# Optimization experiments

Measured on AMD Instinct MI355X. Metric: run time of the kernel, lower is better.

## Reference

```python
import jax, jax.numpy as jnp
import numpy as np

MIX_TIME = 20
NUM_SAMPLES = 128
NUM_ONES = 64


def setup_inputs() -> dict:
    key = jax.random.key(0)
    kz, ka, kw = jax.random.split(key, 3)
    B, D, DZ = 128, 512, 512
    z = (jax.random.uniform(kz, (B, DZ)) < 0.5).astype(jnp.float32)  # conditioned binary vars
    A = jax.random.normal(ka, (D, D), dtype=jnp.float32) * 0.02      # pairwise couplings
    W = jax.random.normal(kw, (D, DZ), dtype=jnp.float32) * 0.02     # w-z couplings
    return {"z": z, "A": A, "W": W}


def reference(z, A, W):
    # Batched conditional double-flip Gibbs sampler.
    # State x: (S, B, D) binary floats; per step pick distinct coords (i, j),
    # evaluate unnormalized log p(w|z) for the 4 value combos, sample categorically.
    S = NUM_SAMPLES
    B, DZ = z.shape
    D = A.shape[0]

    x0 = jnp.zeros((S, B, D), dtype=jnp.float32).at[..., :NUM_ONES].set(1.0)
    cond = jnp.broadcast_to(z[None], (S, B, DZ))  # (S,B,DZ)

    def logp(w):  # quadratic energy: w^T A w + w^T W z  -> (S,B)
        return (jnp.einsum('sbd,de,sbe->sb', w, A, w)
                + jnp.einsum('sbd,dk,sbk->sb', w, W, cond))

    combos = jnp.array([[0., 0.], [0., 1.], [1., 0.], [1., 1.]], dtype=jnp.float32)

    def step(x, k):
        ki, ks = jax.random.split(k)
        ij = jax.random.choice(ki, D, (2,), replace=False)  # distinct i, j
        i, j = ij[0], ij[1]

        def set_ij(v):  # clone x with coords (i,j) set to (v0, v1)
            return x.at[..., i].set(v[0]).at[..., j].set(v[1])

        xs = jax.vmap(set_ij)(combos)                    # (4,S,B,D)
        logits = jnp.moveaxis(jax.vmap(logp)(xs), 0, -1)  # (S,B,4)
        samp = jax.random.categorical(ks, logits)         # (S,B) in {0,1,2,3}
        iv = (samp // 2).astype(x.dtype)
        jv = (samp % 2).astype(x.dtype)
        x = x.at[..., i].set(iv).at[..., j].set(jv)
        return x, None

    keys = jax.random.split(jax.random.key(1), MIX_TIME)
    x, _ = jax.lax.scan(step, x0, keys)
    return x
```

## Files before the change

### kernel.cpp

```cpp
#include <hip/hip_runtime.h>
#include <stdint.h>

#define MIX_TIME 20
#define NCHAIN   16384
#define DDIM     512

#define WS_TBL 0
#define WS_SC  128
#define WS_T0  288
#define WS_U0  800
#define WS_ST0 1312
#define WS_SZ0 1344
#define WS_C   1472

struct U2 { uint32_t a, b; };

__device__ __forceinline__ uint32_t rotl32(uint32_t v, int r) {
  return (v << r) | (v >> (32 - r));
}

__device__ __forceinline__ U2 tf2x32(uint32_t k0, uint32_t k1, uint32_t x0, uint32_t x1) {
  const uint32_t ks2 = k0 ^ k1 ^ 0x1BD11BDAu;
  x0 += k0; x1 += k1;
  x0 += x1; x1 = rotl32(x1, 13); x1 ^= x0;
  x0 += x1; x1 = rotl32(x1, 15); x1 ^= x0;
  x0 += x1; x1 = rotl32(x1, 26); x1 ^= x0;
  x0 += x1; x1 = rotl32(x1,  6); x1 ^= x0;
  x0 += k1; x1 += ks2 + 1u;
  x0 += x1; x1 = rotl32(x1, 17); x1 ^= x0;
  x0 += x1; x1 = rotl32(x1, 29); x1 ^= x0;
  x0 += x1; x1 = rotl32(x1, 16); x1 ^= x0;
  x0 += x1; x1 = rotl32(x1, 24); x1 ^= x0;
  x0 += ks2; x1 += k0 + 2u;
  x0 += x1; x1 = rotl32(x1, 13); x1 ^= x0;
  x0 += x1; x1 = rotl32(x1, 15); x1 ^= x0;
  x0 += x1; x1 = rotl32(x1, 26); x1 ^= x0;
  x0 += x1; x1 = rotl32(x1,  6); x1 ^= x0;
  x0 += k0; x1 += k1 + 3u;
  x0 += x1; x1 = rotl32(x1, 17); x1 ^= x0;
  x0 += x1; x1 = rotl32(x1, 29); x1 ^= x0;
  x0 += x1; x1 = rotl32(x1, 16); x1 ^= x0;
  x0 += x1; x1 = rotl32(x1, 24); x1 ^= x0;
  x0 += k1; x1 += ks2 + 4u;
  x0 += x1; x1 = rotl32(x1, 13); x1 ^= x0;
  x0 += x1; x1 = rotl32(x1, 15); x1 ^= x0;
  x0 += x1; x1 = rotl32(x1, 26); x1 ^= x0;
  x0 += x1; x1 = rotl32(x1,  6); x1 ^= x0;
  x0 += ks2; x1 += k0 + 5u;
  return {x0, x1};
}

__device__ __forceinline__ uint32_t rbits32(uint32_t k0, uint32_t k1, uint32_t m) {
  U2 r = tf2x32(k0, k1, 0u, m);
  return r.a ^ r.b;
}
__device__ __forceinline__ U2 split_key(uint32_t k0, uint32_t k1, uint32_t idx) {
  return tf2x32(k0, k1, 0u, idx);
}

__device__ __forceinline__ float gumbel_from(uint32_t bits) {
  float u = __uint_as_float(0x3f800000u | (bits >> 9)) - 1.0f;
  u = fmaxf(u + 1.17549435e-38f, 1.17549435e-38f);
  return -logf(-logf(u));
}

__device__ __forceinline__ float bpermf(int byteidx, float v) {
  return __int_as_float(__builtin_amdgcn_ds_bpermute(byteidx, __float_as_int(v)));
}
__device__ __forceinline__ uint32_t bpermu(int byteidx, uint32_t v) {
  return (uint32_t)__builtin_amdgcn_ds_bpermute(byteidx, (int)v);
}

__global__ __launch_bounds__(256)
void pre_kernel(const float* __restrict__ A, const float* __restrict__ W,
                const float* __restrict__ z, uint32_t* __restrict__ wsu,
                float* __restrict__ wsf) {
  const int bid = blockIdx.x, tid = threadIdx.x;
  uint32_t* tbl = wsu + WS_TBL;
  uint32_t* sc  = wsu + WS_SC;
  float* T0  = wsf + WS_T0;
  float* U0  = wsf + WS_U0;
  float* St0 = wsf + WS_ST0;
  float* Sz0 = wsf + WS_SZ0;
  float* C   = wsf + WS_C;

  __shared__ float  sred[64];
  __shared__ float4 zs4[8][128];
  __shared__ float  credL[8][64];

  if (bid < MIX_TIME) {
    if (tid >= 64) return;
    const uint32_t t    = (uint32_t)bid;
    const uint32_t lane = (uint32_t)tid;
    const U2 K   = split_key(0u, 1u, t);
    const U2 ki  = split_key(K.a, K.b, 0u);
    const U2 ks  = split_key(K.a, K.b, 1u);
    const U2 sub = split_key(ki.a, ki.b, 1u);

    uint32_t k1 = 0xFFFFFFFFu, m1 = 0xFFFFFFFFu;
    uint32_t k2 = 0xFFFFFFFFu, m2 = 0xFFFFFFFFu;
    #pragma unroll
    for (int p = 0; p < 8; ++p) {
      const uint32_t m   = lane + 64u * (uint32_t)p;
      const uint32_t key = rbits32(sub.a, sub.b, m);
      const bool lt1 = (key < k1) || (key == k1 && m < m1);
      const bool lt2 = (key < k2) || (key == k2 && m < m2);
      if (lt1)      { k2 = k1; m2 = m1; k1 = key; m1 = m; }
      else if (lt2) { k2 = key; m2 = m; }
    }
    #pragma unroll
    for (int msk = 1; msk < 64; msk <<= 1) {
      const uint32_t ok1 = __shfl_xor((int)k1, msk, 64);
      const uint32_t om1 = __shfl_xor((int)m1, msk, 64);
      const uint32_t ok2 = __shfl_xor((int)k2, msk, 64);
      const uint32_t om2 = __shfl_xor((int)m2, msk, 64);
      const bool oless = (ok1 < k1) || (ok1 == k1 && om1 < m1);
      if (oless) {
        const bool l2 = (k1 < ok2) || (k1 == ok2 && m1 < om2);
        const uint32_t nk2 = l2 ? k1 : ok2, nm2 = l2 ? m1 : om2;
        k1 = ok1; m1 = om1; k2 = nk2; m2 = nm2;
      } else {
        const bool l2 = (ok1 < k2) || (ok1 == k2 && om1 < m2);
        if (l2) { k2 = ok1; m2 = om1; }
      }
    }
    if (lane == 0) {
      tbl[4u * t + 0u] = m1;
      tbl[4u * t + 1u] = m2;
      tbl[4u * t + 2u] = ks.a;
      tbl[4u * t + 3u] = ks.b;
      sc[8u * t + 0u] = m1;
      sc[8u * t + 1u] = m2;
      sc[8u * t + 6u] = 0u;
      sc[8u * t + 7u] = 0u;
    }
    if (lane < 4) {
      const uint32_t r = (lane < 2) ? m1 : m2;
      const uint32_t c = (lane & 1) ? m2 : m1;
      sc[8u * t + 2u + lane] = __float_as_uint(A[(size_t)r * DDIM + c]);
    }
    return;
  }

  if (bid <= MIX_TIME + 1) {
    const int e = (bid - MIX_TIME) * 256 + tid;
    float s = 0.f;
    #pragma unroll 1
    for (int d = 0; d < 64; ++d) s += A[(size_t)d * DDIM + e];
    T0[e] = s;
    if (bid == MIX_TIME) {
      if (tid < 64) sred[tid] = s;
      __syncthreads();
      if (tid == 0) {
        float q = 0.f;
        #pragma unroll 1
        for (int e2 = 0; e2 < 64; ++e2) q += sred[e2];
        St0[0] = q;
      }
    }
    return;
  }

  if (bid <= MIX_TIME + 3) {
    const int d = (bid - MIX_TIME - 2) * 256 + tid;
    const float4* Ar = reinterpret_cast<const float4*>(A + (size_t)d * DDIM);
    float s = 0.f;
    #pragma unroll
    for (int k = 0; k < 16; ++k) {
      const float4 v = Ar[k];
      s += v.x; s += v.y; s += v.z; s += v.w;
    }
    U0[d] = s;
    return;
  }

  const int cb = bid - (MIX_TIME + 4);
  const int bg = cb >> 3, slab = cb & 7;
  #pragma unroll
  for (int k = 0; k < 4; ++k) {
    const int idx = tid + 256 * k;
    const int br = idx >> 7, c4i = idx & 127;
    zs4[br][c4i] = reinterpret_cast<const float4*>(z + (size_t)(bg * 8 + br) * DDIM)[c4i];
  }
  __syncthreads();
  const int r = tid & 63;
  const int h = tid >> 6;
  const int d = slab * 64 + r;
  const float4* Wr = reinterpret_cast<const float4*>(W + (size_t)d * DDIM);
  float s0 = 0.f, s1 = 0.f;
  #pragma unroll 4
  for (int k = 0; k < 128; ++k) {
    const float4 w = Wr[k];
    const float4 za = zs4[2 * h][k], zb = zs4[2 * h + 1][k];
    s0 = fmaf(w.x, za.x, s0); s0 = fmaf(w.y, za.y, s0);
    s0 = fmaf(w.z, za.z, s0); s0 = fmaf(w.w, za.w, s0);
    s1 = fmaf(w.x, zb.x, s1); s1 = fmaf(w.y, zb.y, s1);
    s1 = fmaf(w.z, zb.z, s1); s1 = fmaf(w.w, zb.w, s1);
  }
  C[(size_t)(bg * 8 + 2 * h) * DDIM + d]     = s0;
  C[(size_t)(bg * 8 + 2 * h + 1) * DDIM + d] = s1;
  if (slab == 0) { credL[2 * h][r] = s0; credL[2 * h + 1][r] = s1; }
  __syncthreads();
  if (slab == 0 && tid < 8) {
    float s = 0.f;
    #pragma unroll 1
    for (int e = 0; e < 64; ++e) s += credL[tid][e];
    Sz0[bg * 8 + tid] = s;
  }
}

__global__ __launch_bounds__(256)
void gibbs8_kernel(const float* __restrict__ A,
                   const uint32_t* __restrict__ wsu,
                   const float* __restrict__ wsf,
                   float* __restrict__ out) {
  const int tid = threadIdx.x;
  const int l = tid & 63, wv = tid >> 6;
  const uint32_t* tbl = wsu + WS_TBL;
  const uint32_t* sc  = wsu + WS_SC;
  const float* T0w  = wsf + WS_T0;
  const float* U0w  = wsf + WS_U0;
  const float* St0w = wsf + WS_ST0;
  const float* Sz0w = wsf + WS_SZ0;
  const float* Cw   = wsf + WS_C;

  __shared__ __align__(16) float gg[3200];
  __shared__ uint32_t tblL[80];
  if (tid < 80) tblL[tid] = tbl[tid];
  __syncthreads();
  #pragma unroll 1
  for (int p = tid; p < 1600; p += 256) {
    const int r = p / 40, c = p % 40;
    const uint32_t cr = tblL[4 * (r >> 1) + (r & 1)];
    const uint32_t cc = tblL[4 * (c >> 1) + (c & 1)];
    gg[p]        = A[(size_t)cr * DDIM + cc];
    gg[1600 + p] = A[(size_t)cc * DDIM + cr];
  }

  const int ql = l >> 3, qs = l & 7, c4 = l & 3;
  const uint32_t chainbase = ((uint32_t)blockIdx.x * 4u + (uint32_t)wv) * 8u;
  const uint32_t chain_l = chainbase + (uint32_t)ql;
  const uint32_t b_l = chain_l & 127u;
  const uint32_t b_s = (chainbase + (uint32_t)qs) & 127u;
  const float fa  = (float)((c4 >> 1) & 1);
  const float fb  = (float)(c4 & 1);
  const float fab = fa * fb;

  float fTi[3], fTj[3], fUi[3], fUj[3], fci[3], fcj[3], fxi[3], fxj[3];
  uint32_t iiK[3], jjK[3];
  const float* ggb[3];
  #pragma unroll
  for (int k = 0; k < 3; ++k) {
    const int tp = (64 * k + l) >> 3;
    const int tc = (tp < MIX_TIME) ? tp : 0;
    const uint32_t i = sc[8 * tc], j = sc[8 * tc + 1];
    iiK[k] = i; jjK[k] = j;
    fTi[k] = T0w[i];  fTj[k] = T0w[j];
    fUi[k] = U0w[i];  fUj[k] = U0w[j];
    fci[k] = Cw[(size_t)b_s * DDIM + i];
    fcj[k] = Cw[(size_t)b_s * DDIM + j];
    fxi[k] = (i < 64u) ? 1.f : 0.f;
    fxj[k] = (j < 64u) ? 1.f : 0.f;
    ggb[k] = &gg[2 * tc];
  }
  float St = St0w[0];
  float Sz = Sz0w[b_l];
  uint32_t mlo = (qs == 0) ? 0xFFFFFFFFu : 0u;
  uint32_t mhi = mlo;

  float garr[10];
  #pragma unroll
  for (int k = 0; k < 10; ++k) {
    const int f = 64 * k + l;
    const int t = f >> 5;
    const uint32_t qg = ((uint32_t)l & 31u) >> 2;
    const uint32_t m  = (chainbase + qg) * 4u + (uint32_t)(l & 3);
    garr[k] = gumbel_from(rbits32(tbl[4 * t + 2], tbl[4 * t + 3], m));
  }
  __syncthreads();

  const int gvbase = (4 * ql + c4) << 2;
  const int bq4    = ql << 2;

  #pragma unroll
  for (int t = 0; t < MIX_TIME; ++t) {
    const int kS   = t >> 3;
    const int bidx = (((8 * t) & 63) << 2) + bq4;
    const float Ti  = bpermf(bidx, fTi[kS]);
    const float Tj  = bpermf(bidx, fTj[kS]);
    const float Ui  = bpermf(bidx, fUi[kS]);
    const float Uj  = bpermf(bidx, fUj[kS]);
    const float cib = bpermf(bidx, fci[kS]);
    const float cjb = bpermf(bidx, fcj[kS]);
    const float xi  = bpermf(bidx, fxi[kS]);
    const float xj  = bpermf(bidx, fxj[kS]);
    const float gv  = bpermf(gvbase + ((t & 1) << 7), garr[t >> 1]);

    const uint32_t ii = sc[8 * t], jj = sc[8 * t + 1];
    const float Aii = __uint_as_float(sc[8 * t + 2]);
    const float Aij = __uint_as_float(sc[8 * t + 3]);
    const float Aji = __uint_as_float(sc[8 * t + 4]);
    const float Ajj = __uint_as_float(sc[8 * t + 5]);

    const float si   = Ui - xi * Aii - xj * Aij;
    const float sj   = Uj - xi * Aji - xj * Ajj;
    const float sTR  = St - xi * Ti - xj * Tj;
    const float szR  = Sz - xi * cib - xj * cjb;
    const float QR   = sTR - xi * si - xj * sj;
    const float coli = Ti - xi * Aii - xj * Aji;
    const float colj = Tj - xi * Aij - xj * Ajj;
    const float base = QR + szR;
    const float gi   = si + coli + Aii + cib;
    const float gj   = sj + colj + Ajj + cjb;
    const float gij  = Aij + Aji;
    const float v    = gv + (base + fa * gi + fb * gj + fab * gij);

    float bv = v; int bestc = c4;
    #pragma unroll
    for (int msk = 1; msk < 4; msk <<= 1) {
      const float ov = __shfl_xor(bv, msk, 64);
      const int   oc = __shfl_xor(bestc, msk, 64);
      if (ov > bv || (ov == bv && oc < bestc)) { bv = ov; bestc = oc; }
    }

    const int ian = (bestc >> 1) & 1, ibn = bestc & 1;
    const float fan = (float)ian, fbn = (float)ibn;
    const float fdi = fan - xi, fdj = fbn - xj;

    St = St + fdi * Ti + fdj * Tj
            + fdi * (si + fan * Aii + fbn * Aij)
            + fdj * (sj + fan * Aji + fbn * Ajj);
    Sz = Sz + fdi * cib + fdj * cjb;

    const int pk  = ((int)fdi + 1) | (((int)fdj + 1) << 2) | (bestc << 4);
    const int pks = __builtin_amdgcn_ds_bpermute(qs << 5, pk);
    const float fdi_s = (float)((pks & 3) - 1);
    const float fdj_s = (float)(((pks >> 2) & 3) - 1);
    const float fan_s = (float)((pks >> 5) & 1);
    const float fbn_s = (float)((pks >> 4) & 1);

    #pragma unroll
    for (int k = 0; k < 3; ++k) {
      if (t < 8 * k + 7) {
        const float2 ga = *reinterpret_cast<const float2*>(ggb[k] + 80 * t);
        const float2 gB = *reinterpret_cast<const float2*>(ggb[k] + 80 * t + 40);
        const float2 gc = *reinterpret_cast<const float2*>(ggb[k] + 1600 + 80 * t);
        const float2 gd = *reinterpret_cast<const float2*>(ggb[k] + 1600 + 80 * t + 40);
        fTi[k] = fmaf(fdi_s, ga.x, fmaf(fdj_s, gB.x, fTi[k]));
        fTj[k] = fmaf(fdi_s, ga.y, fmaf(fdj_s, gB.y, fTj[k]));
        fUi[k] = fmaf(fdi_s, gc.x, fmaf(fdj_s, gd.x, fUi[k]));
        fUj[k] = fmaf(fdi_s, gc.y, fmaf(fdj_s, gd.y, fUj[k]));
        fxi[k] = (iiK[k] == ii) ? fan_s : fxi[k];
        fxi[k] = (iiK[k] == jj) ? fbn_s : fxi[k];
        fxj[k] = (jjK[k] == ii) ? fan_s : fxj[k];
        fxj[k] = (jjK[k] == jj) ? fbn_s : fxj[k];
      }
    }

    {
      const uint32_t ib = 1u << (ii & 31u);
      const uint32_t nv = (uint32_t)(-(int)ian) & ib;
      const bool own_i = ((uint32_t)qs == (ii >> 6));
      if ((ii >> 5) & 1u) { if (own_i) mhi = (mhi & ~ib) | nv; }
      else                { if (own_i) mlo = (mlo & ~ib) | nv; }
      const uint32_t jb = 1u << (jj & 31u);
      const uint32_t nj = (uint32_t)(-(int)ibn) & jb;
      const bool own_j = ((uint32_t)qs == (jj >> 6));
      if ((jj >> 5) & 1u) { if (own_j) mhi = (mhi & ~jb) | nj; }
      else                { if (own_j) mlo = (mlo & ~jb) | nj; }
    }
  }

  {
    float* wavebase = out + (size_t)chainbase * DDIM;
    #pragma unroll
    for (int g = 0; g < 16; ++g) {
      const int bidx = 16 * g + ((l >> 4) << 2);
      const uint32_t wlo = bpermu(bidx, mlo);
      const uint32_t whi = bpermu(bidx, mhi);
      const uint32_t w   = ((l >> 3) & 1) ? whi : wlo;
      const uint32_t nib = (w >> (4 * (l & 7))) & 0xFu;
      float4 o;
      o.x = (float)( nib       & 1u);
      o.y = (float)((nib >> 1) & 1u);
      o.z = (float)((nib >> 2) & 1u);
      o.w = (float)((nib >> 3) & 1u);
      *reinterpret_cast<float4*>(
          wavebase + (size_t)((g >> 1) * 512 + (64 * (g & 1) + l) * 4)) = o;
    }
  }
}

extern "C" void kernel_launch(void* const* d_in, const int* in_sizes, int n_in,
                              void* d_out, int out_size, void* d_ws, size_t ws_size,
                              hipStream_t stream) {
  const float* z = (const float*)d_in[0];
  const float* A = (const float*)d_in[1];
  const float* W = (const float*)d_in[2];
  float* out = (float*)d_out;
  uint32_t* wsu = (uint32_t*)d_ws;
  float*    wsf = (float*)d_ws;

  hipLaunchKernelGGL(pre_kernel, dim3(MIX_TIME + 4 + 128), dim3(256), 0, stream,
                     A, W, z, wsu, wsf);
  hipLaunchKernelGGL(gibbs8_kernel, dim3(NCHAIN / 32), dim3(256), 0, stream,
                     A, wsu, wsf, out);
}
```

Baseline: 51.87 us.

## Map four chains per wavefront instead of eight to double grid parallelism

Each wavefront now handles 4 chains with 16 lanes per chain instead of 8 chains with 8 lanes per chain, and the grid doubles to NCHAIN/16 blocks. Per-lane state shrinks: two schedule slots instead of three, five gumbel values instead of ten, and one 32-bit mask word per lane instead of two. The output write is remapped accordingly. This raises block count and cuts per-thread serial work and registers, at the cost of redoing the per-block shared-memory table setup from A in twice as many blocks.

```diff
diff --git a/kernel.cpp b/kernel.cpp
--- a/kernel.cpp
+++ b/kernel.cpp
@@ -210,7 +210,7 @@
 }
 
 __global__ __launch_bounds__(256)
-void gibbs8_kernel(const float* __restrict__ A,
+void gibbs4_kernel(const float* __restrict__ A,
                    const uint32_t* __restrict__ wsu,
                    const float* __restrict__ wsf,
                    float* __restrict__ out) {
@@ -237,8 +237,11 @@
     gg[1600 + p] = A[(size_t)cc * DDIM + cr];
   }
 
-  const int ql = l >> 3, qs = l & 7, c4 = l & 3;
-  const uint32_t chainbase = ((uint32_t)blockIdx.x * 4u + (uint32_t)wv) * 8u;
+  const int ql = l >> 4;
+  const int qs = l & 3;
+  const int c4 = l & 3;
+  const int r16 = l & 15;
+  const uint32_t chainbase = ((uint32_t)blockIdx.x * 4u + (uint32_t)wv) * 4u;
   const uint32_t chain_l = chainbase + (uint32_t)ql;
   const uint32_t b_l = chain_l & 127u;
   const uint32_t b_s = (chainbase + (uint32_t)qs) & 127u;
@@ -246,12 +249,12 @@
   const float fb  = (float)(c4 & 1);
   const float fab = fa * fb;
 
-  float fTi[3], fTj[3], fUi[3], fUj[3], fci[3], fcj[3], fxi[3], fxj[3];
-  uint32_t iiK[3], jjK[3];
-  const float* ggb[3];
+  float fTi[2], fTj[2], fUi[2], fUj[2], fci[2], fcj[2], fxi[2], fxj[2];
+  uint32_t iiK[2], jjK[2];
+  const float* ggb[2];
   #pragma unroll
-  for (int k = 0; k < 3; ++k) {
-    const int tp = (64 * k + l) >> 3;
+  for (int k = 0; k < 2; ++k) {
+    const int tp = 16 * k + (l >> 2);
     const int tc = (tp < MIX_TIME) ? tp : 0;
     const uint32_t i = sc[8 * tc], j = sc[8 * tc + 1];
     iiK[k] = i; jjK[k] = j;
@@ -265,27 +268,23 @@
   }
   float St = St0w[0];
   float Sz = Sz0w[b_l];
-  uint32_t mlo = (qs == 0) ? 0xFFFFFFFFu : 0u;
-  uint32_t mhi = mlo;
-
-  float garr[10];
+  uint32_t m32 = (r16 < 2) ? 0xFFFFFFFFu : 0u;
+
+  float garr[5];
   #pragma unroll
-  for (int k = 0; k < 10; ++k) {
+  for (int k = 0; k < 5; ++k) {
     const int f = 64 * k + l;
-    const int t = f >> 5;
-    const uint32_t qg = ((uint32_t)l & 31u) >> 2;
+    const int t = f >> 4;
+    const uint32_t qg = ((uint32_t)l >> 2) & 3u;
     const uint32_t m  = (chainbase + qg) * 4u + (uint32_t)(l & 3);
     garr[k] = gumbel_from(rbits32(tbl[4 * t + 2], tbl[4 * t + 3], m));
   }
   __syncthreads();
 
-  const int gvbase = (4 * ql + c4) << 2;
-  const int bq4    = ql << 2;
-
   #pragma unroll
   for (int t = 0; t < MIX_TIME; ++t) {
-    const int kS   = t >> 3;
-    const int bidx = (((8 * t) & 63) << 2) + bq4;
+    const int kS   = t >> 4;
+    const int bidx = (4 * (t & 15) + ql) << 2;
     const float Ti  = bpermf(bidx, fTi[kS]);
     const float Tj  = bpermf(bidx, fTj[kS]);
     const float Ui  = bpermf(bidx, fUi[kS]);
@@ -294,7 +293,7 @@
     const float cjb = bpermf(bidx, fcj[kS]);
     const float xi  = bpermf(bidx, fxi[kS]);
     const float xj  = bpermf(bidx, fxj[kS]);
-    const float gv  = bpermf(gvbase + ((t & 1) << 7), garr[t >> 1]);
+    const float gv  = bpermf((16 * (t & 3) + 4 * ql + c4) << 2, garr[t >> 2]);
 
     const uint32_t ii = sc[8 * t], jj = sc[8 * t + 1];
     const float Aii = __uint_as_float(sc[8 * t + 2]);
@@ -333,15 +332,15 @@
     Sz = Sz + fdi * cib + fdj * cjb;
 
     const int pk  = ((int)fdi + 1) | (((int)fdj + 1) << 2) | (bestc << 4);
-    const int pks = __builtin_amdgcn_ds_bpermute(qs << 5, pk);
+    const int pks = __builtin_amdgcn_ds_bpermute(qs << 6, pk);
     const float fdi_s = (float)((pks & 3) - 1);
     const float fdj_s = (float)(((pks >> 2) & 3) - 1);
     const float fan_s = (float)((pks >> 5) & 1);
     const float fbn_s = (float)((pks >> 4) & 1);
 
     #pragma unroll
-    for (int k = 0; k < 3; ++k) {
-      if (t < 8 * k + 7) {
+    for (int k = 0; k < 2; ++k) {
+      if (t < 16 * k + 15) {
         const float2 ga = *reinterpret_cast<const float2*>(ggb[k] + 80 * t);
         const float2 gB = *reinterpret_cast<const float2*>(ggb[k] + 80 * t + 40);
         const float2 gc = *reinterpret_cast<const float2*>(ggb[k] + 1600 + 80 * t);
@@ -359,34 +358,29 @@
 
     {
       const uint32_t ib = 1u << (ii & 31u);
-      const uint32_t nv = (uint32_t)(-(int)ian) & ib;
-      const bool own_i = ((uint32_t)qs == (ii >> 6));
-      if ((ii >> 5) & 1u) { if (own_i) mhi = (mhi & ~ib) | nv; }
-      else                { if (own_i) mlo = (mlo & ~ib) | nv; }
+      if ((uint32_t)r16 == (ii >> 5))
+        m32 = (m32 & ~ib) | ((uint32_t)(-(int)ian) & ib);
       const uint32_t jb = 1u << (jj & 31u);
-      const uint32_t nj = (uint32_t)(-(int)ibn) & jb;
-      const bool own_j = ((uint32_t)qs == (jj >> 6));
-      if ((jj >> 5) & 1u) { if (own_j) mhi = (mhi & ~jb) | nj; }
-      else                { if (own_j) mlo = (mlo & ~jb) | nj; }
+      if ((uint32_t)r16 == (jj >> 5))
+        m32 = (m32 & ~jb) | ((uint32_t)(-(int)ibn) & jb);
     }
   }
 
   {
-    float* wavebase = out + (size_t)chainbase * DDIM;
-    #pragma unroll
-    for (int g = 0; g < 16; ++g) {
-      const int bidx = 16 * g + ((l >> 4) << 2);
-      const uint32_t wlo = bpermu(bidx, mlo);
-      const uint32_t whi = bpermu(bidx, mhi);
-      const uint32_t w   = ((l >> 3) & 1) ? whi : wlo;
-      const uint32_t nib = (w >> (4 * (l & 7))) & 0xFu;
+    float4* wavebase = reinterpret_cast<float4*>(out + (size_t)chainbase * DDIM);
+    #pragma unroll
+    for (int g = 0; g < 8; ++g) {
+      const int f  = 64 * g + l;
+      const int e4 = f & 127;
+      const int owner = 16 * (f >> 7) + (e4 >> 3);
+      const uint32_t w = bpermu(owner << 2, m32);
+      const uint32_t nib = (w >> (4 * (e4 & 7))) & 0xFu;
       float4 o;
       o.x = (float)( nib       & 1u);
       o.y = (float)((nib >> 1) & 1u);
       o.z = (float)((nib >> 2) & 1u);
       o.w = (float)((nib >> 3) & 1u);
-      *reinterpret_cast<float4*>(
-          wavebase + (size_t)((g >> 1) * 512 + (64 * (g & 1) + l) * 4)) = o;
+      wavebase[f] = o;
     }
   }
 }
@@ -403,6 +397,6 @@
 
   hipLaunchKernelGGL(pre_kernel, dim3(MIX_TIME + 4 + 128), dim3(256), 0, stream,
                      A, W, z, wsu, wsf);
-  hipLaunchKernelGGL(gibbs8_kernel, dim3(NCHAIN / 32), dim3(256), 0, stream,
+  hipLaunchKernelGGL(gibbs4_kernel, dim3(NCHAIN / 16), dim3(256), 0, stream,
                      A, wsu, wsf, out);
 }
```

Result: slower. 91.73 us (+76.9%).

## Remap lanes so each lane evaluates all four combos for its chain

Applied to the files above, without the earlier changes.

Lanes now own one chain's state per 8-lane group with a segment index, instead of one lane per combo. Each lane computes all four combo logits and takes the argmax serially. This removes the xor-shuffle reduction and the post-decision bpermute broadcast of flip deltas. In exchange it adds four gumbel bpermutes per step and a different mapping for the per-segment precomputed T/U/C values.

```diff
diff --git a/kernel.cpp b/kernel.cpp
--- a/kernel.cpp
+++ b/kernel.cpp
@@ -237,35 +237,32 @@
     gg[1600 + p] = A[(size_t)cc * DDIM + cr];
   }
 
-  const int ql = l >> 3, qs = l & 7, c4 = l & 3;
+  const int ql  = l >> 3;
+  const int seg = l & 7;
   const uint32_t chainbase = ((uint32_t)blockIdx.x * 4u + (uint32_t)wv) * 8u;
   const uint32_t chain_l = chainbase + (uint32_t)ql;
   const uint32_t b_l = chain_l & 127u;
-  const uint32_t b_s = (chainbase + (uint32_t)qs) & 127u;
-  const float fa  = (float)((c4 >> 1) & 1);
-  const float fb  = (float)(c4 & 1);
-  const float fab = fa * fb;
 
   float fTi[3], fTj[3], fUi[3], fUj[3], fci[3], fcj[3], fxi[3], fxj[3];
   uint32_t iiK[3], jjK[3];
   const float* ggb[3];
   #pragma unroll
   for (int k = 0; k < 3; ++k) {
-    const int tp = (64 * k + l) >> 3;
+    const int tp = 8 * k + seg;
     const int tc = (tp < MIX_TIME) ? tp : 0;
     const uint32_t i = sc[8 * tc], j = sc[8 * tc + 1];
     iiK[k] = i; jjK[k] = j;
     fTi[k] = T0w[i];  fTj[k] = T0w[j];
     fUi[k] = U0w[i];  fUj[k] = U0w[j];
-    fci[k] = Cw[(size_t)b_s * DDIM + i];
-    fcj[k] = Cw[(size_t)b_s * DDIM + j];
+    fci[k] = Cw[(size_t)b_l * DDIM + i];
+    fcj[k] = Cw[(size_t)b_l * DDIM + j];
     fxi[k] = (i < 64u) ? 1.f : 0.f;
     fxj[k] = (j < 64u) ? 1.f : 0.f;
     ggb[k] = &gg[2 * tc];
   }
   float St = St0w[0];
   float Sz = Sz0w[b_l];
-  uint32_t mlo = (qs == 0) ? 0xFFFFFFFFu : 0u;
+  uint32_t mlo = (seg == 0) ? 0xFFFFFFFFu : 0u;
   uint32_t mhi = mlo;
 
   float garr[10];
@@ -279,13 +276,10 @@
   }
   __syncthreads();
 
-  const int gvbase = (4 * ql + c4) << 2;
-  const int bq4    = ql << 2;
-
   #pragma unroll
   for (int t = 0; t < MIX_TIME; ++t) {
-    const int kS   = t >> 3;
-    const int bidx = (((8 * t) & 63) << 2) + bq4;
+    const int kS = t >> 3;
+    const int bidx = ((l & 0x38) + (t & 7)) << 2;
     const float Ti  = bpermf(bidx, fTi[kS]);
     const float Tj  = bpermf(bidx, fTj[kS]);
     const float Ui  = bpermf(bidx, fUi[kS]);
@@ -294,7 +288,11 @@
     const float cjb = bpermf(bidx, fcj[kS]);
     const float xi  = bpermf(bidx, fxi[kS]);
     const float xj  = bpermf(bidx, fxj[kS]);
-    const float gv  = bpermf(gvbase + ((t & 1) << 7), garr[t >> 1]);
+    const int gq = ((t & 1) << 7) + (ql << 4);
+    const float gv0 = bpermf(gq + 0,  garr[t >> 1]);
+    const float gv1 = bpermf(gq + 4,  garr[t >> 1]);
+    const float gv2 = bpermf(gq + 8,  garr[t >> 1]);
+    const float gv3 = bpermf(gq + 12, garr[t >> 1]);
 
     const uint32_t ii = sc[8 * t], jj = sc[8 * t + 1];
     const float Aii = __uint_as_float(sc[8 * t + 2]);
@@ -313,15 +311,16 @@
     const float gi   = si + coli + Aii + cib;
     const float gj   = sj + colj + Ajj + cjb;
     const float gij  = Aij + Aji;
-    const float v    = gv + (base + fa * gi + fb * gj + fab * gij);
-
-    float bv = v; int bestc = c4;
-    #pragma unroll
-    for (int msk = 1; msk < 4; msk <<= 1) {
-      const float ov = __shfl_xor(bv, msk, 64);
-      const int   oc = __shfl_xor(bestc, msk, 64);
-      if (ov > bv || (ov == bv && oc < bestc)) { bv = ov; bestc = oc; }
-    }
+
+    const float v0 = gv0 + base;
+    const float v1 = gv1 + (base + gj);
+    const float v2 = gv2 + (base + gi);
+    const float v3 = gv3 + (base + gi + gj + gij);
+
+    int bestc = 0; float bv = v0;
+    if (v1 > bv) { bv = v1; bestc = 1; }
+    if (v2 > bv) { bv = v2; bestc = 2; }
+    if (v3 > bv) { bv = v3; bestc = 3; }
 
     const int ian = (bestc >> 1) & 1, ibn = bestc & 1;
     const float fan = (float)ian, fbn = (float)ibn;
@@ -331,13 +330,6 @@
             + fdi * (si + fan * Aii + fbn * Aij)
             + fdj * (sj + fan * Aji + fbn * Ajj);
     Sz = Sz + fdi * cib + fdj * cjb;
-
-    const int pk  = ((int)fdi + 1) | (((int)fdj + 1) << 2) | (bestc << 4);
-    const int pks = __builtin_amdgcn_ds_bpermute(qs << 5, pk);
-    const float fdi_s = (float)((pks & 3) - 1);
-    const float fdj_s = (float)(((pks >> 2) & 3) - 1);
-    const float fan_s = (float)((pks >> 5) & 1);
-    const float fbn_s = (float)((pks >> 4) & 1);
 
     #pragma unroll
     for (int k = 0; k < 3; ++k) {
@@ -346,26 +338,26 @@
         const float2 gB = *reinterpret_cast<const float2*>(ggb[k] + 80 * t + 40);
         const float2 gc = *reinterpret_cast<const float2*>(ggb[k] + 1600 + 80 * t);
         const float2 gd = *reinterpret_cast<const float2*>(ggb[k] + 1600 + 80 * t + 40);
-        fTi[k] = fmaf(fdi_s, ga.x, fmaf(fdj_s, gB.x, fTi[k]));
-        fTj[k] = fmaf(fdi_s, ga.y, fmaf(fdj_s, gB.y, fTj[k]));
-        fUi[k] = fmaf(fdi_s, gc.x, fmaf(fdj_s, gd.x, fUi[k]));
-        fUj[k] = fmaf(fdi_s, gc.y, fmaf(fdj_s, gd.y, fUj[k]));
-        fxi[k] = (iiK[k] == ii) ? fan_s : fxi[k];
-        fxi[k] = (iiK[k] == jj) ? fbn_s : fxi[k];
-        fxj[k] = (jjK[k] == ii) ? fan_s : fxj[k];
-        fxj[k] = (jjK[k] == jj) ? fbn_s : fxj[k];
+        fTi[k] = fmaf(fdi, ga.x, fmaf(fdj, gB.x, fTi[k]));
+        fTj[k] = fmaf(fdi, ga.y, fmaf(fdj, gB.y, fTj[k]));
+        fUi[k] = fmaf(fdi, gc.x, fmaf(fdj, gd.x, fUi[k]));
+        fUj[k] = fmaf(fdi, gc.y, fmaf(fdj, gd.y, fUj[k]));
+        fxi[k] = (iiK[k] == ii) ? fan : fxi[k];
+        fxi[k] = (iiK[k] == jj) ? fbn : fxi[k];
+        fxj[k] = (jjK[k] == ii) ? fan : fxj[k];
+        fxj[k] = (jjK[k] == jj) ? fbn : fxj[k];
       }
     }
 
     {
       const uint32_t ib = 1u << (ii & 31u);
       const uint32_t nv = (uint32_t)(-(int)ian) & ib;
-      const bool own_i = ((uint32_t)qs == (ii >> 6));
+      const bool own_i = ((uint32_t)seg == (ii >> 6));
       if ((ii >> 5) & 1u) { if (own_i) mhi = (mhi & ~ib) | nv; }
       else                { if (own_i) mlo = (mlo & ~ib) | nv; }
       const uint32_t jb = 1u << (jj & 31u);
       const uint32_t nj = (uint32_t)(-(int)ibn) & jb;
-      const bool own_j = ((uint32_t)qs == (jj >> 6));
+      const bool own_j = ((uint32_t)seg == (jj >> 6));
       if ((jj >> 5) & 1u) { if (own_j) mhi = (mhi & ~jb) | nj; }
       else                { if (own_j) mlo = (mlo & ~jb) | nj; }
     }
```

After: 49.20 us. -5.1%, faster.
